# Optimization experiments

Hardware: AMD Instinct MI355X
Metric: run time of the kernel (lower is better)

Reference implementation:

```python
import jax, jax.numpy as jnp
import numpy as np

NUM_HEADS = 16
NEG_BIG = 1e9


def setup_inputs() -> dict:
    key = jax.random.key(0)
    k1, k2, k3 = jax.random.split(key, 3)
    B, T, D = 2, 2048, 1024
    x = jax.random.normal(k1, (B, T, D), dtype=jnp.float32)
    W_attn = jax.random.normal(k2, (D, 3 * D), dtype=jnp.float32) * 0.02
    b_attn = jnp.zeros((3 * D,), dtype=jnp.float32)
    W_proj = jax.random.normal(k3, (D, D), dtype=jnp.float32) * 0.02
    b_proj = jnp.zeros((D,), dtype=jnp.float32)
    return {"x": x, "W_attn": W_attn, "b_attn": b_attn, "W_proj": W_proj, "b_proj": b_proj}


def reference(x, W_attn, b_attn, W_proj, b_proj):
    B, T, D = x.shape
    H = NUM_HEADS
    dh = D // H
    # qkv projection (GPT-style Conv1D == linear)
    qkv = jnp.einsum('btd,de->bte', x, W_attn) + b_attn  # [B,T,3D]
    q, k, v = jnp.split(qkv, 3, axis=-1)
    # split heads -> [B,H,T,dh]
    q = q.reshape(B, T, H, dh).transpose(0, 2, 1, 3)
    k = k.reshape(B, T, H, dh).transpose(0, 2, 1, 3)
    v = v.reshape(B, T, H, dh).transpose(0, 2, 1, 3)
    # scores [B,H,T,T]; scale=True divides by sqrt(head_dim)
    w = jnp.einsum('bhqd,bhkd->bhqk', q, k) / jnp.sqrt(jnp.float32(dh))
    # causal mask: multiplicative tril then large additive negative, as in source
    mask = jnp.tril(jnp.ones((T, T), dtype=w.dtype))[None, None, :, :]
    w = w * mask - NEG_BIG * (1.0 - mask)
    p = jax.nn.softmax(w, axis=-1)  # attn dropout = identity (eval mode)
    out = jnp.einsum('bhqk,bhkd->bhqd', p, v)  # [B,H,T,dh]
    out = out.transpose(0, 2, 1, 3).reshape(B, T, D)  # merge heads
    out = jnp.einsum('btd,de->bte', out, W_proj) + b_proj  # residual dropout = identity
    return out
```

## Files before the change

kernel.cpp:

```cpp
#include <hip/hip_runtime.h>

typedef unsigned short u16;
typedef unsigned u32;
typedef __bf16 bf16x8 __attribute__((ext_vector_type(8)));
typedef __bf16 bf16x2 __attribute__((ext_vector_type(2)));
typedef float f32x4 __attribute__((ext_vector_type(4)));
typedef u16 u16x4 __attribute__((ext_vector_type(4)));
typedef u32 u32x2 __attribute__((ext_vector_type(2)));
typedef u32 u32x4 __attribute__((ext_vector_type(4)));

__device__ __forceinline__ u16 f2bf(float f) {
  u32 u = __float_as_uint(f);
  u += 0x7fffu + ((u >> 16) & 1u);
  return (u16)(u >> 16);
}

__device__ __forceinline__ u32 pk2(float a, float b) {
#if __has_builtin(__builtin_amdgcn_cvt_pk_bf16_f32)
  bf16x2 r = __builtin_amdgcn_cvt_pk_bf16_f32(a, b);
  return __builtin_bit_cast(u32, r);
#else
  return (u32)f2bf(a) | ((u32)f2bf(b) << 16);
#endif
}

__device__ __forceinline__ float fast_exp2(float x) {
  return __builtin_amdgcn_exp2f(x);
}

__device__ __forceinline__ void gload16(const u16* g, u16* l) {
  __builtin_amdgcn_global_load_lds((__attribute__((address_space(1))) void*)g,
                                   (__attribute__((address_space(3))) void*)l,
                                   16, 0, 0);
}

__global__ __launch_bounds__(256) void cvt_f32_bf16(const float* __restrict__ in,
                                                    u16* __restrict__ out, int n4) {
  int i = blockIdx.x * 256 + threadIdx.x;
  if (i >= n4) return;
  float4 v = ((const float4*)in)[i];
  u16x4 o = { f2bf(v.x), f2bf(v.y), f2bf(v.z), f2bf(v.w) };
  ((u16x4*)out)[i] = o;
}

__global__ __launch_bounds__(256) void transpose_cvt(const float* __restrict__ in,
                                                     u16* __restrict__ out, int R, int C) {
  __shared__ float tile[32][33];
  int c0 = blockIdx.x * 32, r0 = blockIdx.y * 32;
  int tx = threadIdx.x & 31, ty = threadIdx.x >> 5;
#pragma unroll
  for (int i = 0; i < 32; i += 8)
    tile[ty + i][tx] = in[(size_t)(r0 + ty + i) * C + c0 + tx];
  __syncthreads();
#pragma unroll
  for (int i = 0; i < 32; i += 8)
    out[(size_t)(c0 + ty + i) * R + r0 + tx] = f2bf(tile[tx][ty + i]);
}

template <int EPI>
__global__ __launch_bounds__(256) void gemm_bt(const u16* __restrict__ A,
                                               const u16* __restrict__ Bt, int K,
                                               const float* __restrict__ bias,
                                               float* __restrict__ outF,
                                               u16* __restrict__ qb, u16* __restrict__ kb,
                                               u16* __restrict__ vtb) {
  __shared__ __align__(16) u16 As[128 * 32];
  __shared__ __align__(16) u16 Bs[128 * 32];
  const int tid = threadIdx.x;
  const int w = tid >> 6, lane = tid & 63, quad = lane >> 4, l16 = lane & 15;
  const int wm = w >> 1, wn = w & 1;
  const int tm = blockIdx.y * 128, tn = blockIdx.x * 128;

  f32x4 acc[4][4] = {};

  const int ra = lane >> 2;
  const int ca = (lane & 3) * 8;
  const u16* gA0 = A + (size_t)(tm + w * 16 + ra) * K + ca;
  const u16* gA1 = A + (size_t)(tm + (w + 4) * 16 + ra) * K + ca;
  const u16* gB0 = Bt + (size_t)(tn + w * 16 + ra) * K + ca;
  const u16* gB1 = Bt + (size_t)(tn + (w + 4) * 16 + ra) * K + ca;
  u16* lA0 = &As[(w * 16) * 32];
  u16* lA1 = &As[((w + 4) * 16) * 32];
  u16* lB0 = &Bs[(w * 16) * 32];
  u16* lB1 = &Bs[((w + 4) * 16) * 32];

  for (int k0 = 0; k0 < K; k0 += 32) {
    gload16(gA0 + k0, lA0);
    gload16(gA1 + k0, lA1);
    gload16(gB0 + k0, lB0);
    gload16(gB1 + k0, lB1);
    __syncthreads();
    bf16x8 af[4], bfr[4];
#pragma unroll
    for (int mt = 0; mt < 4; ++mt)
      af[mt] = *(const bf16x8*)&As[(wm * 64 + mt * 16 + l16) * 32 + quad * 8];
#pragma unroll
    for (int nt = 0; nt < 4; ++nt)
      bfr[nt] = *(const bf16x8*)&Bs[(wn * 64 + nt * 16 + l16) * 32 + quad * 8];
#pragma unroll
    for (int mt = 0; mt < 4; ++mt)
#pragma unroll
      for (int nt = 0; nt < 4; ++nt)
        acc[mt][nt] = __builtin_amdgcn_mfma_f32_16x16x32_bf16(af[mt], bfr[nt], acc[mt][nt], 0, 0, 0);
    __syncthreads();
  }

#pragma unroll
  for (int mt = 0; mt < 4; ++mt) {
#pragma unroll
    for (int nt = 0; nt < 4; ++nt) {
      const int row0 = tm + wm * 64 + mt * 16 + quad * 4;
      const int col = tn + wn * 64 + nt * 16 + l16;
      float v4[4];
#pragma unroll
      for (int r = 0; r < 4; ++r) v4[r] = acc[mt][nt][r] + bias[col];
      if (EPI == 0) {
        int which = col >> 10, d = col & 1023, hh = d >> 6, dd = d & 63;
        int b = row0 >> 11, t = row0 & 2047;
        int bh = (b << 4) + hh;
        if (which == 0) {
#pragma unroll
          for (int r = 0; r < 4; ++r)
            qb[((size_t)bh * 2048 + t + r) * 64 + dd] = f2bf(v4[r] * 0.18033688f);
        } else if (which == 1) {
#pragma unroll
          for (int r = 0; r < 4; ++r)
            kb[((size_t)bh * 2048 + t + r) * 64 + dd] = f2bf(v4[r]);
        } else {
          u16x4 pk = { f2bf(v4[0]), f2bf(v4[1]), f2bf(v4[2]), f2bf(v4[3]) };
          *(u16x4*)(vtb + ((size_t)bh * 64 + dd) * 2048 + t) = pk;
        }
      } else {
#pragma unroll
        for (int r = 0; r < 4; ++r)
          outF[(size_t)(row0 + r) * 1024 + col] = v4[r];
      }
    }
  }
}

__global__ __launch_bounds__(256) void flash_attn(const u16* __restrict__ qb,
                                                  const u16* __restrict__ kb,
                                                  const u16* __restrict__ vtb,
                                                  u16* __restrict__ ao) {
  const int T = 2048;
  const int tid = threadIdx.x;
  const int w = tid >> 6, lane = tid & 63;
  const int quad = lane >> 4, l16 = lane & 15;
  const int bx = blockIdx.x;
  const int bh = bx & 31;
  const int g0 = bx >> 5;
  const int G = (g0 & 24) | (((g0 >> 3) & 1) ? (7 - (g0 & 7)) : (g0 & 7));
  const int b = bh >> 4, h = bh & 15;
  const int ro = w * 16 + l16;
  const int qrow = G * 64 + ro;
  const size_t kvbase = (size_t)bh * T * 64;
  const int nkt = G + 1;

  __shared__ __align__(16) u16 Ks[64][72];
  __shared__ __align__(16) u16 Vs[64][72];
  __shared__ __align__(16) u16 Ps[4][16][72];

  bf16x8 q0 = *(const bf16x8*)(qb + kvbase + (size_t)qrow * 64 + quad * 8);
  bf16x8 q1 = *(const bf16x8*)(qb + kvbase + (size_t)qrow * 64 + 32 + quad * 8);

  bf16x8 ones;
#pragma unroll
  for (int i = 0; i < 8; ++i) ones[i] = (__bf16)1.0f;

  f32x4 o[4] = {};
  f32x4 o_lp = {};

  const int tok = tid >> 2, c4 = (tid & 3) * 16;
  const u16* kg = kb + kvbase + (size_t)tok * 64 + c4;
  const u16* vg = vtb + (size_t)(bh * 64 + tok) * 2048 + c4;

  {
    u32x4 a0 = *(const u32x4*)(kg);
    u32x4 a1 = *(const u32x4*)(kg + 8);
    u32x4 b0 = *(const u32x4*)(vg);
    u32x4 b1 = *(const u32x4*)(vg + 8);
    *(u32x4*)&Ks[tok][c4] = a0;  *(u32x4*)&Ks[tok][c4 + 8] = a1;
    *(u32x4*)&Vs[tok][c4] = b0;  *(u32x4*)&Vs[tok][c4 + 8] = b1;
  }
  __syncthreads();

  u32x4 sk0, sk1, sv0, sv1;

  for (int kt = 0; kt < nkt; ++kt) {
    const bool more = (kt + 1 < nkt);
    if (more) {
      const int kb2 = (kt + 1) * 64;
      sk0 = *(const u32x4*)(kg + (size_t)kb2 * 64);
      sk1 = *(const u32x4*)(kg + (size_t)kb2 * 64 + 8);
      sv0 = *(const u32x4*)(vg + kb2);
      sv1 = *(const u32x4*)(vg + kb2 + 8);
    }

    f32x4 z[4];
#pragma unroll
    for (int st = 0; st < 4; ++st) {
      bf16x8 kf0 = *(const bf16x8*)&Ks[st * 16 + l16][quad * 8];
      bf16x8 kf1 = *(const bf16x8*)&Ks[st * 16 + l16][32 + quad * 8];
      f32x4 zz = {};
      zz = __builtin_amdgcn_mfma_f32_16x16x32_bf16(kf0, q0, zz, 0, 0, 0);
      zz = __builtin_amdgcn_mfma_f32_16x16x32_bf16(kf1, q1, zz, 0, 0, 0);
      z[st] = zz;
    }
    if (kt == nkt - 1) {
#pragma unroll
      for (int st = 0; st < 4; ++st)
#pragma unroll
        for (int r = 0; r < 4; ++r)
          if (st * 16 + quad * 4 + r > ro) z[st][r] = -1e30f;
    }
#pragma unroll
    for (int st = 0; st < 4; ++st) {
      float p0 = fast_exp2(z[st][0]), p1 = fast_exp2(z[st][1]);
      float p2 = fast_exp2(z[st][2]), p3 = fast_exp2(z[st][3]);
      u32x2 pw = { pk2(p0, p1), pk2(p2, p3) };
      *(u32x2*)&Ps[w][l16][st * 16 + quad * 4] = pw;
    }

    bf16x8 pf0 = *(const bf16x8*)&Ps[w][l16][quad * 8];
    bf16x8 pf1 = *(const bf16x8*)&Ps[w][l16][32 + quad * 8];
    o_lp = __builtin_amdgcn_mfma_f32_16x16x32_bf16(ones, pf0, o_lp, 0, 0, 0);
    o_lp = __builtin_amdgcn_mfma_f32_16x16x32_bf16(ones, pf1, o_lp, 0, 0, 0);
#pragma unroll
    for (int dt = 0; dt < 4; ++dt) {
      bf16x8 vf0 = *(const bf16x8*)&Vs[dt * 16 + l16][quad * 8];
      bf16x8 vf1 = *(const bf16x8*)&Vs[dt * 16 + l16][32 + quad * 8];
      o[dt] = __builtin_amdgcn_mfma_f32_16x16x32_bf16(vf0, pf0, o[dt], 0, 0, 0);
      o[dt] = __builtin_amdgcn_mfma_f32_16x16x32_bf16(vf1, pf1, o[dt], 0, 0, 0);
    }

    __syncthreads();
    if (more) {
      *(u32x4*)&Ks[tok][c4] = sk0;  *(u32x4*)&Ks[tok][c4 + 8] = sk1;
      *(u32x4*)&Vs[tok][c4] = sv0;  *(u32x4*)&Vs[tok][c4 + 8] = sv1;
    }
    __syncthreads();
  }

  float inv = 1.0f / o_lp[0];
  size_t obase = ((size_t)b * T + qrow) * 1024 + h * 64;
#pragma unroll
  for (int dt = 0; dt < 4; ++dt) {
    u16x4 ov = { f2bf(o[dt][0] * inv), f2bf(o[dt][1] * inv),
                 f2bf(o[dt][2] * inv), f2bf(o[dt][3] * inv) };
    *(u16x4*)(ao + obase + dt * 16 + quad * 4) = ov;
  }
}

extern "C" void kernel_launch(void* const* d_in, const int* in_sizes, int n_in,
                              void* d_out, int out_size, void* d_ws, size_t ws_size,
                              hipStream_t stream) {
  const float* x      = (const float*)d_in[0];
  const float* W_attn = (const float*)d_in[1];
  const float* b_attn = (const float*)d_in[2];
  const float* W_proj = (const float*)d_in[3];
  const float* b_proj = (const float*)d_in[4];
  float* out = (float*)d_out;

  if (ws_size < 50331648u) return;

  char* ws = (char*)d_ws;
  u16* xb  = (u16*)(ws);
  u16* wat = (u16*)(ws + 8388608u);
  u16* wpt = (u16*)(ws + 14680064u);
  u16* qb  = (u16*)(ws + 16777216u);
  u16* kb  = (u16*)(ws + 25165824u);
  u16* vtb = (u16*)(ws + 33554432u);
  u16* ao  = (u16*)(ws + 41943040u);

  cvt_f32_bf16<<<4096, 256, 0, stream>>>(x, xb, 4194304 / 4);
  transpose_cvt<<<dim3(96, 32), 256, 0, stream>>>(W_attn, wat, 1024, 3072);
  transpose_cvt<<<dim3(32, 32), 256, 0, stream>>>(W_proj, wpt, 1024, 1024);

  gemm_bt<0><<<dim3(24, 32), 256, 0, stream>>>(xb, wat, 1024, b_attn, nullptr, qb, kb, vtb);

  flash_attn<<<dim3(1024), 256, 0, stream>>>(qb, kb, vtb, ao);

  gemm_bt<1><<<dim3(8, 32), 256, 0, stream>>>(ao, wpt, 1024, b_proj, out, nullptr, nullptr, nullptr);
}
```

Measured before the change: 194.3 us.

## Load K and V MFMA fragments directly from global memory, dropping LDS staging

Removes the shared-memory K/V tiles, register prefetch and both per-iteration block barriers, and has each wave read its K and V^T fragments straight from global memory. This is meant to eliminate LDS store/load traffic and __syncthreads stalls. In exchange the four waves in a block each fetch the same K/V data redundantly through the caches, and the global-load latency is no longer hidden by software prefetch.

```diff
diff --git a/kernel.cpp b/kernel.cpp
--- a/kernel.cpp
+++ b/kernel.cpp
@@ -157,8 +157,6 @@
   const size_t kvbase = (size_t)bh * T * 64;
   const int nkt = G + 1;
 
-  __shared__ __align__(16) u16 Ks[64][72];
-  __shared__ __align__(16) u16 Vs[64][72];
   __shared__ __align__(16) u16 Ps[4][16][72];
 
   bf16x8 q0 = *(const bf16x8*)(qb + kvbase + (size_t)qrow * 64 + quad * 8);
@@ -171,37 +169,15 @@
   f32x4 o[4] = {};
   f32x4 o_lp = {};
 
-  const int tok = tid >> 2, c4 = (tid & 3) * 16;
-  const u16* kg = kb + kvbase + (size_t)tok * 64 + c4;
-  const u16* vg = vtb + (size_t)(bh * 64 + tok) * 2048 + c4;
-
-  {
-    u32x4 a0 = *(const u32x4*)(kg);
-    u32x4 a1 = *(const u32x4*)(kg + 8);
-    u32x4 b0 = *(const u32x4*)(vg);
-    u32x4 b1 = *(const u32x4*)(vg + 8);
-    *(u32x4*)&Ks[tok][c4] = a0;  *(u32x4*)&Ks[tok][c4 + 8] = a1;
-    *(u32x4*)&Vs[tok][c4] = b0;  *(u32x4*)&Vs[tok][c4 + 8] = b1;
-  }
-  __syncthreads();
-
-  u32x4 sk0, sk1, sv0, sv1;
+  const u16* kp = kb + kvbase + (size_t)l16 * 64 + quad * 8;
+  const u16* vp = vtb + ((size_t)bh * 64 + l16) * 2048 + quad * 8;
 
   for (int kt = 0; kt < nkt; ++kt) {
-    const bool more = (kt + 1 < nkt);
-    if (more) {
-      const int kb2 = (kt + 1) * 64;
-      sk0 = *(const u32x4*)(kg + (size_t)kb2 * 64);
-      sk1 = *(const u32x4*)(kg + (size_t)kb2 * 64 + 8);
-      sv0 = *(const u32x4*)(vg + kb2);
-      sv1 = *(const u32x4*)(vg + kb2 + 8);
-    }
-
     f32x4 z[4];
 #pragma unroll
     for (int st = 0; st < 4; ++st) {
-      bf16x8 kf0 = *(const bf16x8*)&Ks[st * 16 + l16][quad * 8];
-      bf16x8 kf1 = *(const bf16x8*)&Ks[st * 16 + l16][32 + quad * 8];
+      bf16x8 kf0 = *(const bf16x8*)(kp + st * 1024);
+      bf16x8 kf1 = *(const bf16x8*)(kp + st * 1024 + 32);
       f32x4 zz = {};
       zz = __builtin_amdgcn_mfma_f32_16x16x32_bf16(kf0, q0, zz, 0, 0, 0);
       zz = __builtin_amdgcn_mfma_f32_16x16x32_bf16(kf1, q1, zz, 0, 0, 0);
@@ -228,18 +204,14 @@
     o_lp = __builtin_amdgcn_mfma_f32_16x16x32_bf16(ones, pf1, o_lp, 0, 0, 0);
 #pragma unroll
     for (int dt = 0; dt < 4; ++dt) {
-      bf16x8 vf0 = *(const bf16x8*)&Vs[dt * 16 + l16][quad * 8];
-      bf16x8 vf1 = *(const bf16x8*)&Vs[dt * 16 + l16][32 + quad * 8];
+      bf16x8 vf0 = *(const bf16x8*)(vp + (size_t)dt * 32768);
+      bf16x8 vf1 = *(const bf16x8*)(vp + (size_t)dt * 32768 + 32);
       o[dt] = __builtin_amdgcn_mfma_f32_16x16x32_bf16(vf0, pf0, o[dt], 0, 0, 0);
       o[dt] = __builtin_amdgcn_mfma_f32_16x16x32_bf16(vf1, pf1, o[dt], 0, 0, 0);
     }
 
-    __syncthreads();
-    if (more) {
-      *(u32x4*)&Ks[tok][c4] = sk0;  *(u32x4*)&Ks[tok][c4 + 8] = sk1;
-      *(u32x4*)&Vs[tok][c4] = sv0;  *(u32x4*)&Vs[tok][c4 + 8] = sv1;
-    }
-    __syncthreads();
+    kp += 4096;
+    vp += 64;
   }
 
   float inv = 1.0f / o_lp[0];
```

Result: slower. 276.4 us (+42.3%).

## Merge prep kernels, deepen GEMM K-step, split-K output projection

Applied to the files above, without the earlier changes.

Fuses the x conversion and the two weight transpose-conversions into a single launch. Both GEMMs now load two 32-wide K slices per barrier pair, halving syncs per K. The output projection (only 256 blocks) is split along K into two halves that write fp32 partials, reusing the dead q buffer as scratch, and a final reduce kernel adds the partials and bias. This gives more blocks to fill the CUs, at the cost of extra fp32 partial traffic and one more launch.

```diff
diff --git a/kernel.cpp b/kernel.cpp
--- a/kernel.cpp
+++ b/kernel.cpp
@@ -34,19 +34,26 @@
                                    16, 0, 0);
 }
 
-__global__ __launch_bounds__(256) void cvt_f32_bf16(const float* __restrict__ in,
-                                                    u16* __restrict__ out, int n4) {
-  int i = blockIdx.x * 256 + threadIdx.x;
-  if (i >= n4) return;
-  float4 v = ((const float4*)in)[i];
-  u16x4 o = { f2bf(v.x), f2bf(v.y), f2bf(v.z), f2bf(v.w) };
-  ((u16x4*)out)[i] = o;
-}
-
-__global__ __launch_bounds__(256) void transpose_cvt(const float* __restrict__ in,
-                                                     u16* __restrict__ out, int R, int C) {
+__global__ __launch_bounds__(256) void prep(const float* __restrict__ x,
+                                            u16* __restrict__ xb,
+                                            const float* __restrict__ Wa,
+                                            u16* __restrict__ wat,
+                                            const float* __restrict__ Wp,
+                                            u16* __restrict__ wpt) {
   __shared__ float tile[32][33];
-  int c0 = blockIdx.x * 32, r0 = blockIdx.y * 32;
+  const int bid = blockIdx.x;
+  if (bid < 4096) {
+    int i = bid * 256 + threadIdx.x;
+    float4 v = ((const float4*)x)[i];
+    u16x4 o = { f2bf(v.x), f2bf(v.y), f2bf(v.z), f2bf(v.w) };
+    ((u16x4*)xb)[i] = o;
+    return;
+  }
+  const float* in; u16* out; int C, bx, by;
+  if (bid < 7168) { int id = bid - 4096; bx = id % 96; by = id / 96; in = Wa; out = wat; C = 3072; }
+  else            { int id = bid - 7168; bx = id & 31; by = id >> 5; in = Wp; out = wpt; C = 1024; }
+  const int R = 1024;
+  int c0 = bx * 32, r0 = by * 32;
   int tx = threadIdx.x & 31, ty = threadIdx.x >> 5;
 #pragma unroll
   for (int i = 0; i < 32; i += 8)
@@ -57,15 +64,15 @@
     out[(size_t)(c0 + ty + i) * R + r0 + tx] = f2bf(tile[tx][ty + i]);
 }
 
-template <int EPI>
-__global__ __launch_bounds__(256) void gemm_bt(const u16* __restrict__ A,
-                                               const u16* __restrict__ Bt, int K,
-                                               const float* __restrict__ bias,
-                                               float* __restrict__ outF,
-                                               u16* __restrict__ qb, u16* __restrict__ kb,
-                                               u16* __restrict__ vtb) {
-  __shared__ __align__(16) u16 As[128 * 32];
-  __shared__ __align__(16) u16 Bs[128 * 32];
+__global__ __launch_bounds__(256) void gemm_qkv(const u16* __restrict__ A,
+                                                const u16* __restrict__ Bt,
+                                                const float* __restrict__ bias,
+                                                u16* __restrict__ qb,
+                                                u16* __restrict__ kb,
+                                                u16* __restrict__ vtb) {
+  const int K = 1024;
+  __shared__ __align__(16) u16 As[2][128 * 32];
+  __shared__ __align__(16) u16 Bs[2][128 * 32];
   const int tid = threadIdx.x;
   const int w = tid >> 6, lane = tid & 63, quad = lane >> 4, l16 = lane & 15;
   const int wm = w >> 1, wn = w & 1;
@@ -79,29 +86,35 @@
   const u16* gA1 = A + (size_t)(tm + (w + 4) * 16 + ra) * K + ca;
   const u16* gB0 = Bt + (size_t)(tn + w * 16 + ra) * K + ca;
   const u16* gB1 = Bt + (size_t)(tn + (w + 4) * 16 + ra) * K + ca;
-  u16* lA0 = &As[(w * 16) * 32];
-  u16* lA1 = &As[((w + 4) * 16) * 32];
-  u16* lB0 = &Bs[(w * 16) * 32];
-  u16* lB1 = &Bs[((w + 4) * 16) * 32];
-
-  for (int k0 = 0; k0 < K; k0 += 32) {
-    gload16(gA0 + k0, lA0);
-    gload16(gA1 + k0, lA1);
-    gload16(gB0 + k0, lB0);
-    gload16(gB1 + k0, lB1);
-    __syncthreads();
-    bf16x8 af[4], bfr[4];
-#pragma unroll
-    for (int mt = 0; mt < 4; ++mt)
-      af[mt] = *(const bf16x8*)&As[(wm * 64 + mt * 16 + l16) * 32 + quad * 8];
-#pragma unroll
-    for (int nt = 0; nt < 4; ++nt)
-      bfr[nt] = *(const bf16x8*)&Bs[(wn * 64 + nt * 16 + l16) * 32 + quad * 8];
-#pragma unroll
-    for (int mt = 0; mt < 4; ++mt)
+
+  for (int k0 = 0; k0 < K; k0 += 64) {
+#pragma unroll
+    for (int h = 0; h < 2; ++h) {
+      u16* lA0 = &As[h][(w * 16) * 32];
+      u16* lA1 = &As[h][((w + 4) * 16) * 32];
+      u16* lB0 = &Bs[h][(w * 16) * 32];
+      u16* lB1 = &Bs[h][((w + 4) * 16) * 32];
+      gload16(gA0 + k0 + h * 32, lA0);
+      gload16(gA1 + k0 + h * 32, lA1);
+      gload16(gB0 + k0 + h * 32, lB0);
+      gload16(gB1 + k0 + h * 32, lB1);
+    }
+    __syncthreads();
+#pragma unroll
+    for (int h = 0; h < 2; ++h) {
+      bf16x8 af[4], bfr[4];
+#pragma unroll
+      for (int mt = 0; mt < 4; ++mt)
+        af[mt] = *(const bf16x8*)&As[h][(wm * 64 + mt * 16 + l16) * 32 + quad * 8];
 #pragma unroll
       for (int nt = 0; nt < 4; ++nt)
-        acc[mt][nt] = __builtin_amdgcn_mfma_f32_16x16x32_bf16(af[mt], bfr[nt], acc[mt][nt], 0, 0, 0);
+        bfr[nt] = *(const bf16x8*)&Bs[h][(wn * 64 + nt * 16 + l16) * 32 + quad * 8];
+#pragma unroll
+      for (int mt = 0; mt < 4; ++mt)
+#pragma unroll
+        for (int nt = 0; nt < 4; ++nt)
+          acc[mt][nt] = __builtin_amdgcn_mfma_f32_16x16x32_bf16(af[mt], bfr[nt], acc[mt][nt], 0, 0, 0);
+    }
     __syncthreads();
   }
 
@@ -114,29 +127,102 @@
       float v4[4];
 #pragma unroll
       for (int r = 0; r < 4; ++r) v4[r] = acc[mt][nt][r] + bias[col];
-      if (EPI == 0) {
-        int which = col >> 10, d = col & 1023, hh = d >> 6, dd = d & 63;
-        int b = row0 >> 11, t = row0 & 2047;
-        int bh = (b << 4) + hh;
-        if (which == 0) {
-#pragma unroll
-          for (int r = 0; r < 4; ++r)
-            qb[((size_t)bh * 2048 + t + r) * 64 + dd] = f2bf(v4[r] * 0.18033688f);
-        } else if (which == 1) {
-#pragma unroll
-          for (int r = 0; r < 4; ++r)
-            kb[((size_t)bh * 2048 + t + r) * 64 + dd] = f2bf(v4[r]);
-        } else {
-          u16x4 pk = { f2bf(v4[0]), f2bf(v4[1]), f2bf(v4[2]), f2bf(v4[3]) };
-          *(u16x4*)(vtb + ((size_t)bh * 64 + dd) * 2048 + t) = pk;
-        }
+      int which = col >> 10, d = col & 1023, hh = d >> 6, dd = d & 63;
+      int b = row0 >> 11, t = row0 & 2047;
+      int bh = (b << 4) + hh;
+      if (which == 0) {
+#pragma unroll
+        for (int r = 0; r < 4; ++r)
+          qb[((size_t)bh * 2048 + t + r) * 64 + dd] = f2bf(v4[r] * 0.18033688f);
+      } else if (which == 1) {
+#pragma unroll
+        for (int r = 0; r < 4; ++r)
+          kb[((size_t)bh * 2048 + t + r) * 64 + dd] = f2bf(v4[r]);
       } else {
-#pragma unroll
-        for (int r = 0; r < 4; ++r)
-          outF[(size_t)(row0 + r) * 1024 + col] = v4[r];
+        u16x4 pk = { f2bf(v4[0]), f2bf(v4[1]), f2bf(v4[2]), f2bf(v4[3]) };
+        *(u16x4*)(vtb + ((size_t)bh * 64 + dd) * 2048 + t) = pk;
       }
     }
   }
+}
+
+__global__ __launch_bounds__(256) void gemm_psk(const u16* __restrict__ A,
+                                                const u16* __restrict__ Bt,
+                                                float* __restrict__ P0,
+                                                float* __restrict__ P1) {
+  const int K = 1024;
+  __shared__ __align__(16) u16 As[2][128 * 32];
+  __shared__ __align__(16) u16 Bs[2][128 * 32];
+  const int tid = threadIdx.x;
+  const int w = tid >> 6, lane = tid & 63, quad = lane >> 4, l16 = lane & 15;
+  const int wm = w >> 1, wn = w & 1;
+  const int tm = blockIdx.y * 128, tn = blockIdx.x * 128;
+  const int kz = blockIdx.z;
+  float* dst = kz ? P1 : P0;
+  const int kbase = kz * 512;
+
+  f32x4 acc[4][4] = {};
+
+  const int ra = lane >> 2;
+  const int ca = (lane & 3) * 8;
+  const u16* gA0 = A + (size_t)(tm + w * 16 + ra) * K + kbase + ca;
+  const u16* gA1 = A + (size_t)(tm + (w + 4) * 16 + ra) * K + kbase + ca;
+  const u16* gB0 = Bt + (size_t)(tn + w * 16 + ra) * K + kbase + ca;
+  const u16* gB1 = Bt + (size_t)(tn + (w + 4) * 16 + ra) * K + kbase + ca;
+
+  for (int k0 = 0; k0 < 512; k0 += 64) {
+#pragma unroll
+    for (int h = 0; h < 2; ++h) {
+      u16* lA0 = &As[h][(w * 16) * 32];
+      u16* lA1 = &As[h][((w + 4) * 16) * 32];
+      u16* lB0 = &Bs[h][(w * 16) * 32];
+      u16* lB1 = &Bs[h][((w + 4) * 16) * 32];
+      gload16(gA0 + k0 + h * 32, lA0);
+      gload16(gA1 + k0 + h * 32, lA1);
+      gload16(gB0 + k0 + h * 32, lB0);
+      gload16(gB1 + k0 + h * 32, lB1);
+    }
+    __syncthreads();
+#pragma unroll
+    for (int h = 0; h < 2; ++h) {
+      bf16x8 af[4], bfr[4];
+#pragma unroll
+      for (int mt = 0; mt < 4; ++mt)
+        af[mt] = *(const bf16x8*)&As[h][(wm * 64 + mt * 16 + l16) * 32 + quad * 8];
+#pragma unroll
+      for (int nt = 0; nt < 4; ++nt)
+        bfr[nt] = *(const bf16x8*)&Bs[h][(wn * 64 + nt * 16 + l16) * 32 + quad * 8];
+#pragma unroll
+      for (int mt = 0; mt < 4; ++mt)
+#pragma unroll
+        for (int nt = 0; nt < 4; ++nt)
+          acc[mt][nt] = __builtin_amdgcn_mfma_f32_16x16x32_bf16(af[mt], bfr[nt], acc[mt][nt], 0, 0, 0);
+    }
+    __syncthreads();
+  }
+
+#pragma unroll
+  for (int mt = 0; mt < 4; ++mt) {
+#pragma unroll
+    for (int nt = 0; nt < 4; ++nt) {
+      const int row0 = tm + wm * 64 + mt * 16 + quad * 4;
+      const int col = tn + wn * 64 + nt * 16 + l16;
+#pragma unroll
+      for (int r = 0; r < 4; ++r)
+        dst[(size_t)(row0 + r) * 1024 + col] = acc[mt][nt][r];
+    }
+  }
+}
+
+__global__ __launch_bounds__(256) void reduce_bias(const float* __restrict__ P,
+                                                   float* __restrict__ out,
+                                                   const float* __restrict__ bias) {
+  int i = blockIdx.x * 256 + threadIdx.x;
+  float4 a = ((const float4*)out)[i];
+  float4 b = ((const float4*)P)[i];
+  float4 c = ((const float4*)bias)[i & 255];
+  float4 r = { a.x + b.x + c.x, a.y + b.y + c.y, a.z + b.z + c.z, a.w + b.w + c.w };
+  ((float4*)out)[i] = r;
 }
 
 __global__ __launch_bounds__(256) void flash_attn(const u16* __restrict__ qb,
@@ -272,14 +358,15 @@
   u16* kb  = (u16*)(ws + 25165824u);
   u16* vtb = (u16*)(ws + 33554432u);
   u16* ao  = (u16*)(ws + 41943040u);
-
-  cvt_f32_bf16<<<4096, 256, 0, stream>>>(x, xb, 4194304 / 4);
-  transpose_cvt<<<dim3(96, 32), 256, 0, stream>>>(W_attn, wat, 1024, 3072);
-  transpose_cvt<<<dim3(32, 32), 256, 0, stream>>>(W_proj, wpt, 1024, 1024);
-
-  gemm_bt<0><<<dim3(24, 32), 256, 0, stream>>>(xb, wat, 1024, b_attn, nullptr, qb, kb, vtb);
+  float* Pp = (float*)(ws + 16777216u);
+
+  prep<<<8192, 256, 0, stream>>>(x, xb, W_attn, wat, W_proj, wpt);
+
+  gemm_qkv<<<dim3(24, 32), 256, 0, stream>>>(xb, wat, b_attn, qb, kb, vtb);
 
   flash_attn<<<dim3(1024), 256, 0, stream>>>(qb, kb, vtb, ao);
 
-  gemm_bt<1><<<dim3(8, 32), 256, 0, stream>>>(ao, wpt, 1024, b_proj, out, nullptr, nullptr, nullptr);
-}
+  gemm_psk<<<dim3(8, 32, 2), 256, 0, stream>>>(ao, wpt, Pp, out);
+
+  reduce_bias<<<4096, 256, 0, stream>>>(Pp, out, b_proj);
+}
```

Measured after the change: 190.6 us. No clear change (-1.9%).
